# Optimization experiments

Measured on AMD Instinct MI355X. Metric: run time of the kernel, lower is better.

## Reference

```python
import jax, jax.numpy as jnp
import numpy as np

B, S, E, D = 256, 256, 2, 128  # batch, seq_len, encoder_dim, decoder_dim


def setup_inputs() -> dict:
    key = jax.random.key(0)
    ks = jax.random.split(key, 9)
    u = lambda k, shape, n: jax.random.uniform(k, shape, jnp.float32, -1.0 / np.sqrt(n), 1.0 / np.sqrt(n))
    return {
        "out_encoder": jax.random.normal(ks[0], (B, S, E), jnp.float32),
        "W1_w": u(ks[1], (S, S), S),            # Linear(seq_len, seq_len)
        "W1_b": u(ks[2], (S,), S),
        "W2_w": u(ks[3], (S, 2 * S), 2 * S),    # Linear(2*seq_len, seq_len)
        "W2_b": u(ks[4], (S,), 2 * S),
        "W_ih": u(ks[5], (4 * D, E), D),        # LSTMCell input weights (i,f,g,o)
        "W_hh": u(ks[6], (4 * D, D), D),
        "b_ih": u(ks[7], (4 * D,), D),
        "b_hh": u(ks[8], (4 * D,), D),
    }


def reference(out_encoder, W1_w, W1_b, W2_w, W2_b, W_ih, W_hh, b_ih, b_hh):
    b, s, e = out_encoder.shape
    d = W_hh.shape[1]
    dt = out_encoder.dtype

    # W_2 term: encoder flattened to [B, 2S]; identical every step, hoist it.
    w2term = out_encoder.reshape(b, s * e) @ W2_w.T + W2_b          # [B, S]
    # W_1 applied to a row of S copies of h_d equals h_d * rowsum(W1) + b.
    w1sum = W1_w.sum(axis=1)                                        # [S]

    def attn(h):  # h: [B, D] -> context [B, E]
        hterm = h[:, :, None] * w1sum[None, None, :] + W1_b         # [B, D, S]
        en = jnp.tanh(w2term[:, None, :] + hterm)                   # [B, D, S]
        alpha = jax.nn.softmax(en, axis=-1).mean(axis=1)            # [B, S] (softmax over seq)
        return jnp.einsum('bs,bse->be', alpha, out_encoder)         # [B, E]

    def lstm_cell(x, h, c):
        gates = x @ W_ih.T + h @ W_hh.T + b_ih + b_hh               # [B, 4D]
        i, f, g, o = jnp.split(gates, 4, axis=-1)
        c = jax.nn.sigmoid(f) * c + jax.nn.sigmoid(i) * jnp.tanh(g)
        h = jax.nn.sigmoid(o) * jnp.tanh(c)
        return h, c

    h0 = jnp.zeros((b, d), dt)
    c0 = jnp.zeros((b, d), dt)

    def step(carry, _):
        h, c = carry
        x = attn(h)
        h, c = lstm_cell(x, h, c)
        return (h, c), h

    _, hs = jax.lax.scan(step, (h0, c0), None, length=s)
    return hs  # [S, B, D]: stacked decoder hidden states (original returns a list of h_t)
```

## Files before the change

### kernel.cpp

```cpp
#include <hip/hip_runtime.h>

#define NB 256
#define NS 256
#define NE 2
#define ND 128
#define NT 256
#define NN 16

typedef float vf4 __attribute__((ext_vector_type(4)));
typedef _Float16 f16x8 __attribute__((ext_vector_type(8)));
typedef float f32x4 __attribute__((ext_vector_type(4)));

constexpr float L2E = 1.4426950408889634f;
constexpr float PI_F = 3.14159265358979323846f;

__device__ const float CT[16][16] = {
 {1,0,0,0,0,0,0,0,0,0,0,0,0,0,0,0},
 {0,1,0,0,0,0,0,0,0,0,0,0,0,0,0,0},
 {-1,0,2,0,0,0,0,0,0,0,0,0,0,0,0,0},
 {0,-3,0,4,0,0,0,0,0,0,0,0,0,0,0,0},
 {1,0,-8,0,8,0,0,0,0,0,0,0,0,0,0,0},
 {0,5,0,-20,0,16,0,0,0,0,0,0,0,0,0,0},
 {-1,0,18,0,-48,0,32,0,0,0,0,0,0,0,0,0},
 {0,-7,0,56,0,-112,0,64,0,0,0,0,0,0,0,0},
 {1,0,-32,0,160,0,-256,0,128,0,0,0,0,0,0,0},
 {0,9,0,-120,0,432,0,-576,0,256,0,0,0,0,0},
 {-1,0,50,0,-400,0,1120,0,-1280,0,512,0,0,0,0,0},
 {0,-11,0,220,0,-1232,0,2816,0,-2816,0,1024,0,0,0,0},
 {1,0,-72,0,840,0,-3584,0,6912,0,-6144,0,2048,0,0,0},
 {0,13,0,-364,0,2912,0,-9984,0,16640,0,-13312,0,4096,0,0},
 {-1,0,98,0,-1568,0,9408,0,-26880,0,39424,0,-28672,0,8192,0},
 {0,-15,0,560,0,-6048,0,28800,0,-70400,0,92160,0,-61440,0,16384}};

template <int C>
__device__ __forceinline__ float dppadd(float x) {
    return x + __builtin_bit_cast(float,
        __builtin_amdgcn_update_dpp(0, __builtin_bit_cast(int, x), C, 0xF, 0xF, true));
}
__device__ __forceinline__ float red_quad(float x) {
    x = dppadd<0xB1>(x); x = dppadd<0x4E>(x); return x;
}
__device__ __forceinline__ float red_wave64(float x) {
    x = dppadd<0xB1>(x); x = dppadd<0x4E>(x); x = dppadd<0x141>(x);
    x = dppadd<0x140>(x); x = dppadd<0x142>(x); x = dppadd<0x143>(x); return x;
}
__device__ __forceinline__ float red16_all(float x) {
    x = dppadd<0xB1>(x);
    x = dppadd<0x4E>(x);
    x = dppadd<0x141>(x);
    x = dppadd<0x140>(x);
    return x;
}

__global__ __launch_bounds__(NT, 1)
void attn_lstm_decoder(const float* __restrict__ enc,
                       const float* __restrict__ W1w,
                       const float* __restrict__ W1b,
                       const float* __restrict__ W2w,
                       const float* __restrict__ W2b,
                       const float* __restrict__ Wih,
                       const float* __restrict__ Whh,
                       const float* __restrict__ bih,
                       const float* __restrict__ bhh,
                       float* __restrict__ out)
{
    const int b    = blockIdx.x;
    const int t    = threadIdx.x;
    const int wave = t >> 6;
    const int lane = t & 63;
    const int grp  = lane >> 4;
    const int nib  = lane & 15;
    const int sub  = grp & 1;
    const int cpy  = grp >> 1;
    const int gl   = 32 * wave + 16 * sub + nib;

    __shared__ __align__(16) _Float16 hist16[2 * ND];
    __shared__ __align__(16) float xwbuf[2][8];
    __shared__ float A2_l[NS];
    __shared__ float g2_l[NS];
    __shared__ float e0_l[NS];
    __shared__ float e1_l[NS];
    __shared__ float Ml[NN * NN];
    __shared__ float2 Pn[NN];
    __shared__ float2 Vl[NN];
    __shared__ float Pm0[NN], Pm1[NN];

    #pragma unroll
    for (int i = t; i < NS * NE; i += NT) {
        float v = enc[b * (NS * NE) + i];
        if (i & 1) e1_l[i >> 1] = v; else e0_l[i >> 1] = v;
    }
    {
        const int mi = t >> 4, mj = t & 15;
        const float w = (mi == 0) ? (1.0f / NN) : (2.0f / NN);
        Ml[t] = w * __cosf((float)(mi * (2 * mj + 1)) * (PI_F / (2 * NN)));
    }
    __syncthreads();

    for (int r = 0; r < 64; ++r) {
        const int s = wave * 64 + r;
        float p = W1w[s * NS + lane]       + W1w[s * NS + lane + 64]
                + W1w[s * NS + lane + 128] + W1w[s * NS + lane + 192];
        p = red_wave64(p);
        if (lane == 63) g2_l[s] = p * (2.0f * L2E);
        float qq = 0.0f;
        #pragma unroll
        for (int kk = 0; kk < 8; ++kk) {
            const int c = lane + kk * 64;
            const float ev = (c & 1) ? e1_l[c >> 1] : e0_l[c >> 1];
            qq = fmaf(ev, W2w[s * (2 * NS) + c], qq);
        }
        qq = red_wave64(qq);
        if (lane == 63) A2_l[s] = (qq + W2b[s] + W1b[s]) * (2.0f * L2E);
    }
    __syncthreads();

    {
        const int jn = 4 * wave + grp;
        const float y  = __cosf((float)(2 * jn + 1) * (PI_F / (2 * NN)));
        const float C2 = -2.0f * L2E;
        float l = 0.0f, p0 = 0.0f, p1 = 0.0f;
        #pragma unroll
        for (int k = 0; k < 16; ++k) {
            const int s = k * 16 + nib;
            const float m1 = fmaf(y, g2_l[s], A2_l[s]);
            const float u  = __builtin_amdgcn_exp2f(m1);
            const float rc = __builtin_amdgcn_rcpf(u + 1.0f);
            const float e  = __builtin_amdgcn_exp2f(rc * C2);
            l += e;
            p0 = fmaf(e, e0_l[s], p0);
            p1 = fmaf(e, e1_l[s], p1);
        }
        l = red16_all(l); p0 = red16_all(p0); p1 = red16_all(p1);
        if (nib == 0) {
            const float rl = __builtin_amdgcn_rcpf(l);
            Pn[jn] = make_float2(p0 * rl, p1 * rl);
        }
    }
    __syncthreads();

    if (t < NN) {
        float v0 = 0.0f, v1 = 0.0f;
        #pragma unroll
        for (int j = 0; j < NN; ++j) {
            v0 = fmaf(Ml[t * NN + j], Pn[j].x, v0);
            v1 = fmaf(Ml[t * NN + j], Pn[j].y, v1);
        }
        Vl[t] = make_float2(v0 * (1.0f / ND), v1 * (1.0f / ND));
    }

    f16x8 wf[4][2][4];
    #pragma unroll
    for (int j = 0; j < 4; ++j) {
        #pragma unroll
        for (int s = 0; s < 2; ++s) {
            const int row = 128 * j + 32 * wave + 16 * s + nib;
            #pragma unroll
            for (int kt = 0; kt < 4; ++kt) {
                const vf4 wa = *reinterpret_cast<const vf4*>(Whh + row * ND + 32 * kt + 8 * grp);
                const vf4 wb = *reinterpret_cast<const vf4*>(Whh + row * ND + 32 * kt + 8 * grp + 4);
                f16x8 wv;
                wv[0] = (_Float16)wa.x; wv[1] = (_Float16)wa.y;
                wv[2] = (_Float16)wa.z; wv[3] = (_Float16)wa.w;
                wv[4] = (_Float16)wb.x; wv[5] = (_Float16)wb.y;
                wv[6] = (_Float16)wb.z; wv[7] = (_Float16)wb.w;
                wf[j][s][kt] = wv;
            }
        }
    }
    float wi0_[4], wi1_[4], bb_[4];
    #pragma unroll
    for (int j = 0; j < 4; ++j) {
        const int r = 128 * j + gl;
        wi0_[j] = Wih[r * 2 + 0];
        wi1_[j] = Wih[r * 2 + 1];
        bb_[j]  = bih[r] + bhh[r];
    }

    if (t < 2 * ND) hist16[t] = (_Float16)0.0f;
    float h_reg = 0.0f, c_reg = 0.0f;
    __syncthreads();

    if (t < NN) {
        float s0 = 0.0f, s1 = 0.0f;
        #pragma unroll
        for (int k = 0; k < NN; ++k) {
            s0 = fmaf(Vl[k].x, CT[k][t], s0);
            s1 = fmaf(Vl[k].y, CT[k][t], s1);
        }
        Pm0[t] = s0; Pm1[t] = s1;
    }
    __syncthreads();

    float cc0[8], cc1[8];
    #pragma unroll
    for (int i = 0; i < 8; ++i) {
        cc0[i] = Pm0[2 * i + cpy];
        cc1[i] = Pm1[2 * i + cpy];
    }

    auto phaseG = [&](float h, int pw) {
        const float h2 = h * h;
        float v0 = cc0[7], v1 = cc1[7];
        #pragma unroll
        for (int k = 6; k >= 0; --k) {
            v0 = fmaf(v0, h2, cc0[k]);
            v1 = fmaf(v1, h2, cc1[k]);
        }
        const float hsel = cpy ? h : 1.0f;
        v0 *= hsel;
        v1 *= hsel;
        v0 = red_wave64(v0); v1 = red_wave64(v1);
        if (lane == 63) {
            xwbuf[pw][2 * wave + 0] = v0;
            xwbuf[pw][2 * wave + 1] = v1;
        }
    };

    phaseG(0.0f, 0);
    __syncthreads();

    for (int step = 0; step < NS; ++step) {
        const int pr = step & 1;
        const int rs = pr ^ 1;
        const int ws = pr;
        const _Float16* hb = &hist16[rs * ND];

        const f16x8 af0 = __builtin_bit_cast(f16x8, *reinterpret_cast<const int4*>(hb + 0  + 8 * grp));
        const f16x8 af1 = __builtin_bit_cast(f16x8, *reinterpret_cast<const int4*>(hb + 32 + 8 * grp));
        const f16x8 af2 = __builtin_bit_cast(f16x8, *reinterpret_cast<const int4*>(hb + 64 + 8 * grp));
        const f16x8 af3 = __builtin_bit_cast(f16x8, *reinterpret_cast<const int4*>(hb + 96 + 8 * grp));

        float2 xv = *reinterpret_cast<const float2*>(&xwbuf[pr][2 * (lane & 3)]);
        const float x0 = red_quad(xv.x);
        const float x1 = red_quad(xv.y);
        float bt[4];
        #pragma unroll
        for (int j = 0; j < 4; ++j)
            bt[j] = fmaf(x0, wi0_[j], fmaf(x1, wi1_[j], bb_[j]));

        float ga[4];
        #pragma unroll
        for (int j = 0; j < 4; ++j) {
            f32x4 a0 = {0.0f, 0.0f, 0.0f, 0.0f};
            f32x4 a1 = {0.0f, 0.0f, 0.0f, 0.0f};
            a0 = __builtin_amdgcn_mfma_f32_16x16x32_f16(af0, wf[j][0][0], a0, 0, 0, 0);
            a1 = __builtin_amdgcn_mfma_f32_16x16x32_f16(af0, wf[j][1][0], a1, 0, 0, 0);
            a0 = __builtin_amdgcn_mfma_f32_16x16x32_f16(af1, wf[j][0][1], a0, 0, 0, 0);
            a1 = __builtin_amdgcn_mfma_f32_16x16x32_f16(af1, wf[j][1][1], a1, 0, 0, 0);
            a0 = __builtin_amdgcn_mfma_f32_16x16x32_f16(af2, wf[j][0][2], a0, 0, 0, 0);
            a1 = __builtin_amdgcn_mfma_f32_16x16x32_f16(af2, wf[j][1][2], a1, 0, 0, 0);
            a0 = __builtin_amdgcn_mfma_f32_16x16x32_f16(af3, wf[j][0][3], a0, 0, 0, 0);
            a1 = __builtin_amdgcn_mfma_f32_16x16x32_f16(af3, wf[j][1][3], a1, 0, 0, 0);
            ga[j] = sub ? a1[0] : a0[0];
        }

        const float gi = ga[0] + bt[0];
        const float gf = ga[1] + bt[1];
        const float gg = ga[2] + bt[2];
        const float go = ga[3] + bt[3];

        const float si = __builtin_amdgcn_rcpf(1.0f + __builtin_amdgcn_exp2f(-L2E * gi));
        const float sf = __builtin_amdgcn_rcpf(1.0f + __builtin_amdgcn_exp2f(-L2E * gf));
        const float so = __builtin_amdgcn_rcpf(1.0f + __builtin_amdgcn_exp2f(-L2E * go));
        const float tg = 1.0f - 2.0f * __builtin_amdgcn_rcpf(
            __builtin_amdgcn_exp2f(2.0f * L2E * gg) + 1.0f);
        c_reg = fmaf(sf, c_reg, si * tg);
        const float tc2 = 1.0f - 2.0f * __builtin_amdgcn_rcpf(
            __builtin_amdgcn_exp2f(2.0f * L2E * c_reg) + 1.0f);
        h_reg = so * tc2;

        if (cpy == 0) {
            hist16[ws * ND + gl] = (_Float16)h_reg;
            out[(size_t)step * (NB * ND) + b * ND + gl] = h_reg;
        }
        phaseG(h_reg, pr ^ 1);

        asm volatile("s_waitcnt lgkmcnt(0)" ::: "memory");
        __builtin_amdgcn_s_barrier();
    }
}

extern "C" void kernel_launch(void* const* d_in, const int* in_sizes, int n_in,
                              void* d_out, int out_size, void* d_ws, size_t ws_size,
                              hipStream_t stream) {
    const float* enc = (const float*)d_in[0];
    const float* W1w = (const float*)d_in[1];
    const float* W1b = (const float*)d_in[2];
    const float* W2w = (const float*)d_in[3];
    const float* W2b = (const float*)d_in[4];
    const float* Wih = (const float*)d_in[5];
    const float* Whh = (const float*)d_in[6];
    const float* bih = (const float*)d_in[7];
    const float* bhh = (const float*)d_in[8];
    attn_lstm_decoder<<<NB, NT, 0, stream>>>(enc, W1w, W1b, W2w, W2b,
                                             Wih, Whh, bih, bhh, (float*)d_out);
}
```

Before: 271.1 us.

## Process two batch rows per block with 512 threads

Packs two batch elements into each workgroup (512 threads, two independent 256-thread halves) and halves the grid. Shared precomputation such as the W1 row sums is done once per block, and the per-row state buffers are duplicated. The intent is to cut per-block setup and raise occupancy per CU. In exchange, the two rows' recurrences now share a block-wide barrier each step, and fewer blocks leave CUs idle on a GPU with many compute units.

```diff
diff --git a/kernel.cpp b/kernel.cpp
--- a/kernel.cpp
+++ b/kernel.cpp
@@ -4,7 +4,8 @@
 #define NS 256
 #define NE 2
 #define ND 128
-#define NT 256
+#define NBB 2
+#define NT 512
 #define NN 16
 
 typedef float vf4 __attribute__((ext_vector_type(4)));
@@ -52,7 +53,7 @@
     return x;
 }
 
-__global__ __launch_bounds__(NT, 1)
+__global__ __launch_bounds__(NT, 2)
 void attn_lstm_decoder(const float* __restrict__ enc,
                        const float* __restrict__ W1w,
                        const float* __restrict__ W1b,
@@ -64,89 +65,94 @@
                        const float* __restrict__ bhh,
                        float* __restrict__ out)
 {
-    const int b    = blockIdx.x;
+    const int b0   = blockIdx.x * NBB;
     const int t    = threadIdx.x;
-    const int wave = t >> 6;
+    const int tb   = t >> 8;
+    const int tt   = t & 255;
+    const int ww   = tt >> 6;
     const int lane = t & 63;
     const int grp  = lane >> 4;
     const int nib  = lane & 15;
     const int sub  = grp & 1;
     const int cpy  = grp >> 1;
-    const int gl   = 32 * wave + 16 * sub + nib;
-
-    __shared__ __align__(16) _Float16 hist16[2 * ND];
-    __shared__ __align__(16) float xwbuf[2][8];
-    __shared__ float A2_l[NS];
+    const int gl   = 32 * ww + 16 * sub + nib;
+    const int b    = b0 + tb;
+
+    __shared__ __align__(16) _Float16 hist16[NBB][2 * ND];
+    __shared__ __align__(16) float xwbuf[NBB][2][8];
+    __shared__ float A2_l[NBB][NS];
+    __shared__ float e0_l[NBB][NS];
+    __shared__ float e1_l[NBB][NS];
     __shared__ float g2_l[NS];
-    __shared__ float e0_l[NS];
-    __shared__ float e1_l[NS];
     __shared__ float Ml[NN * NN];
-    __shared__ float2 Pn[NN];
-    __shared__ float2 Vl[NN];
-    __shared__ float Pm0[NN], Pm1[NN];
+    __shared__ float2 Pn[NBB][NN];
+    __shared__ float2 Vl[NBB][NN];
+    __shared__ float Pm0[NBB][NN], Pm1[NBB][NN];
 
     #pragma unroll
-    for (int i = t; i < NS * NE; i += NT) {
-        float v = enc[b * (NS * NE) + i];
-        if (i & 1) e1_l[i >> 1] = v; else e0_l[i >> 1] = v;
-    }
-    {
-        const int mi = t >> 4, mj = t & 15;
+    for (int i = tt; i < NS * NE; i += 256) {
+        float v = enc[(size_t)b * (NS * NE) + i];
+        if (i & 1) e1_l[tb][i >> 1] = v; else e0_l[tb][i >> 1] = v;
+    }
+    if (tb == 0) {
+        const int mi = tt >> 4, mj = tt & 15;
         const float w = (mi == 0) ? (1.0f / NN) : (2.0f / NN);
-        Ml[t] = w * __cosf((float)(mi * (2 * mj + 1)) * (PI_F / (2 * NN)));
+        Ml[tt] = w * __cosf((float)(mi * (2 * mj + 1)) * (PI_F / (2 * NN)));
     }
     __syncthreads();
 
     for (int r = 0; r < 64; ++r) {
-        const int s = wave * 64 + r;
-        float p = W1w[s * NS + lane]       + W1w[s * NS + lane + 64]
-                + W1w[s * NS + lane + 128] + W1w[s * NS + lane + 192];
-        p = red_wave64(p);
-        if (lane == 63) g2_l[s] = p * (2.0f * L2E);
+        const int s = ww * 64 + r;
+        if (tb == 0) {
+            float p = W1w[s * NS + lane]       + W1w[s * NS + lane + 64]
+                    + W1w[s * NS + lane + 128] + W1w[s * NS + lane + 192];
+            p = red_wave64(p);
+            if (lane == 63) g2_l[s] = p * (2.0f * L2E);
+        }
         float qq = 0.0f;
         #pragma unroll
         for (int kk = 0; kk < 8; ++kk) {
             const int c = lane + kk * 64;
-            const float ev = (c & 1) ? e1_l[c >> 1] : e0_l[c >> 1];
+            const float ev = (c & 1) ? e1_l[tb][c >> 1] : e0_l[tb][c >> 1];
             qq = fmaf(ev, W2w[s * (2 * NS) + c], qq);
         }
         qq = red_wave64(qq);
-        if (lane == 63) A2_l[s] = (qq + W2b[s] + W1b[s]) * (2.0f * L2E);
+        if (lane == 63) A2_l[tb][s] = (qq + W2b[s] + W1b[s]) * (2.0f * L2E);
     }
     __syncthreads();
 
     {
-        const int jn = 4 * wave + grp;
+        const int jn = 4 * ww + grp;
         const float y  = __cosf((float)(2 * jn + 1) * (PI_F / (2 * NN)));
         const float C2 = -2.0f * L2E;
         float l = 0.0f, p0 = 0.0f, p1 = 0.0f;
         #pragma unroll
         for (int k = 0; k < 16; ++k) {
             const int s = k * 16 + nib;
-            const float m1 = fmaf(y, g2_l[s], A2_l[s]);
+            const float m1 = fmaf(y, g2_l[s], A2_l[tb][s]);
             const float u  = __builtin_amdgcn_exp2f(m1);
             const float rc = __builtin_amdgcn_rcpf(u + 1.0f);
             const float e  = __builtin_amdgcn_exp2f(rc * C2);
             l += e;
-            p0 = fmaf(e, e0_l[s], p0);
-            p1 = fmaf(e, e1_l[s], p1);
+            p0 = fmaf(e, e0_l[tb][s], p0);
+            p1 = fmaf(e, e1_l[tb][s], p1);
         }
         l = red16_all(l); p0 = red16_all(p0); p1 = red16_all(p1);
         if (nib == 0) {
             const float rl = __builtin_amdgcn_rcpf(l);
-            Pn[jn] = make_float2(p0 * rl, p1 * rl);
-        }
-    }
-    __syncthreads();
-
-    if (t < NN) {
+            Pn[tb][jn] = make_float2(p0 * rl, p1 * rl);
+        }
+    }
+    __syncthreads();
+
+    if (tt < NN) {
         float v0 = 0.0f, v1 = 0.0f;
         #pragma unroll
         for (int j = 0; j < NN; ++j) {
-            v0 = fmaf(Ml[t * NN + j], Pn[j].x, v0);
-            v1 = fmaf(Ml[t * NN + j], Pn[j].y, v1);
-        }
-        Vl[t] = make_float2(v0 * (1.0f / ND), v1 * (1.0f / ND));
+            v0 = fmaf(Ml[tt * NN + j], Pn[tb][j].x, v0);
+            v1 = fmaf(Ml[tt * NN + j], Pn[tb][j].y, v1);
+        }
+        Vl[tb][tt] = make_float2(v0 * (1.0f / ND), v1 * (1.0f / ND));
     }
 
     f16x8 wf[4][2][4];
@@ -154,7 +160,7 @@
     for (int j = 0; j < 4; ++j) {
         #pragma unroll
         for (int s = 0; s < 2; ++s) {
-            const int row = 128 * j + 32 * wave + 16 * s + nib;
+            const int row = 128 * j + 32 * ww + 16 * s + nib;
             #pragma unroll
             for (int kt = 0; kt < 4; ++kt) {
                 const vf4 wa = *reinterpret_cast<const vf4*>(Whh + row * ND + 32 * kt + 8 * grp);
@@ -177,26 +183,26 @@
         bb_[j]  = bih[r] + bhh[r];
     }
 
-    if (t < 2 * ND) hist16[t] = (_Float16)0.0f;
+    if (tt < 2 * ND) hist16[tb][tt] = (_Float16)0.0f;
     float h_reg = 0.0f, c_reg = 0.0f;
     __syncthreads();
 
-    if (t < NN) {
+    if (tt < NN) {
         float s0 = 0.0f, s1 = 0.0f;
         #pragma unroll
         for (int k = 0; k < NN; ++k) {
-            s0 = fmaf(Vl[k].x, CT[k][t], s0);
-            s1 = fmaf(Vl[k].y, CT[k][t], s1);
-        }
-        Pm0[t] = s0; Pm1[t] = s1;
+            s0 = fmaf(Vl[tb][k].x, CT[k][tt], s0);
+            s1 = fmaf(Vl[tb][k].y, CT[k][tt], s1);
+        }
+        Pm0[tb][tt] = s0; Pm1[tb][tt] = s1;
     }
     __syncthreads();
 
     float cc0[8], cc1[8];
     #pragma unroll
     for (int i = 0; i < 8; ++i) {
-        cc0[i] = Pm0[2 * i + cpy];
-        cc1[i] = Pm1[2 * i + cpy];
+        cc0[i] = Pm0[tb][2 * i + cpy];
+        cc1[i] = Pm1[tb][2 * i + cpy];
     }
 
     auto phaseG = [&](float h, int pw) {
@@ -212,8 +218,8 @@
         v1 *= hsel;
         v0 = red_wave64(v0); v1 = red_wave64(v1);
         if (lane == 63) {
-            xwbuf[pw][2 * wave + 0] = v0;
-            xwbuf[pw][2 * wave + 1] = v1;
+            xwbuf[tb][pw][2 * ww + 0] = v0;
+            xwbuf[tb][pw][2 * ww + 1] = v1;
         }
     };
 
@@ -224,14 +230,14 @@
         const int pr = step & 1;
         const int rs = pr ^ 1;
         const int ws = pr;
-        const _Float16* hb = &hist16[rs * ND];
+        const _Float16* hb = &hist16[tb][rs * ND];
 
         const f16x8 af0 = __builtin_bit_cast(f16x8, *reinterpret_cast<const int4*>(hb + 0  + 8 * grp));
         const f16x8 af1 = __builtin_bit_cast(f16x8, *reinterpret_cast<const int4*>(hb + 32 + 8 * grp));
         const f16x8 af2 = __builtin_bit_cast(f16x8, *reinterpret_cast<const int4*>(hb + 64 + 8 * grp));
         const f16x8 af3 = __builtin_bit_cast(f16x8, *reinterpret_cast<const int4*>(hb + 96 + 8 * grp));
 
-        float2 xv = *reinterpret_cast<const float2*>(&xwbuf[pr][2 * (lane & 3)]);
+        float2 xv = *reinterpret_cast<const float2*>(&xwbuf[tb][pr][2 * (lane & 3)]);
         const float x0 = red_quad(xv.x);
         const float x1 = red_quad(xv.y);
         float bt[4];
@@ -271,8 +277,8 @@
         h_reg = so * tc2;
 
         if (cpy == 0) {
-            hist16[ws * ND + gl] = (_Float16)h_reg;
-            out[(size_t)step * (NB * ND) + b * ND + gl] = h_reg;
+            hist16[tb][ws * ND + gl] = (_Float16)h_reg;
+            out[(size_t)step * (NB * ND) + (size_t)b * ND + gl] = h_reg;
         }
         phaseG(h_reg, pr ^ 1);
 
@@ -293,6 +299,6 @@
     const float* Whh = (const float*)d_in[6];
     const float* bih = (const float*)d_in[7];
     const float* bhh = (const float*)d_in[8];
-    attn_lstm_decoder<<<NB, NT, 0, stream>>>(enc, W1w, W1b, W2w, W2b,
-                                             Wih, Whh, bih, bhh, (float*)d_out);
-}
+    attn_lstm_decoder<<<NB / NBB, NT, 0, stream>>>(enc, W1w, W1b, W2w, W2b,
+                                                   Wih, Whh, bih, bhh, (float*)d_out);
+}
```

Result: slower. 354.9 us (+30.9%).
